# Performance work log

Hardware: AMD Instinct MI355X
Metric: run time of the kernel (lower is better)

The kernel has to match this reference:

```python
import jax, jax.numpy as jnp
import numpy as np

GAMMA = 0.99
LMBDA = 0.95
SHAPE = (8192, 256, 4, 1)  # (batch, steps, agents, 1)


def setup_inputs() -> dict:
    key = jax.random.key(0)
    k1, k2, k3, k4 = jax.random.split(key, 4)
    reward = jax.random.normal(k1, SHAPE, dtype=jnp.float32)
    # sparse binary termination flags (as float, matching terminated.float())
    terminated = (jax.random.uniform(k2, SHAPE) < 0.01).astype(jnp.float32)
    value = jax.random.normal(k3, SHAPE, dtype=jnp.float32)
    next_value = jax.random.normal(k4, SHAPE, dtype=jnp.float32)
    return {"reward": reward, "terminated": terminated,
            "value": value, "next_value": next_value}


def _gae(reward, terminated, value, next_value):
    not_done = 1.0 - terminated
    # delta_t = r_t + gamma * V(s_{t+1}) * not_done_t - V(s_t), all steps at once
    delta = reward + GAMMA * next_value * not_done - value  # (B, T, ...)

    # time-major for the scan: (T, B, ...)
    delta_t = jnp.moveaxis(delta, 1, 0)
    nd_t = jnp.moveaxis(not_done, 1, 0)

    def step(gae, x):
        d, nd = x
        gae = d + GAMMA * LMBDA * nd * gae
        return gae, gae

    init = jnp.zeros(delta_t.shape[1:], dtype=delta.dtype)
    # reverse=True: backward-time recurrence, outputs aligned to original order
    _, adv_t = jax.lax.scan(step, init, (delta_t, nd_t), reverse=True)
    advantages = jnp.moveaxis(adv_t, 0, 1)  # back to (B, T, ...)
    returns = advantages + value
    return advantages, returns


def reference(reward, terminated, value, next_value):
    return _gae(reward, terminated, value, next_value)
```

## Files before the change

kernel.cpp:

```cpp
#include <hip/hip_runtime.h>


#define GAMMA 0.99f
#define LMBDA 0.95f

typedef float f32x4 __attribute__((ext_vector_type(4)));
typedef unsigned char u8;

constexpr float K0 = GAMMA * LMBDA;

__device__ __forceinline__ void issue_loads(
    const f32x4* __restrict__ R4, const f32x4* __restrict__ T4,
    const f32x4* __restrict__ V4, const f32x4* __restrict__ N4,
    int b, int lane, f32x4 r[4], f32x4 tm[4], f32x4 v[4], f32x4 nv[4])
{
#pragma unroll
    for (int q = 0; q < 4; ++q) {
        const int gi = b * 256 + 64 * q + lane;
        r[q]  = R4[gi];
        tm[q] = T4[gi];
        v[q]  = V4[gi];
        nv[q] = N4[gi];
    }
}

__device__ __forceinline__ void phaseA(
    float* __restrict__ D_, u8* __restrict__ C_, int lane,
    const f32x4 r[4], const f32x4 tm[4], const f32x4 nv[4], const f32x4 v[4])
{
#pragma unroll
    for (int q = 0; q < 4; ++q) {
        const int f    = 64 * q + lane;
        const int s    = 255 - f;
        const int row  = s & 15;
        const int col  = (4 * (s >> 4) + 4 * row) & 63;
        const int addr = row * 64 + col;

        f32x4 d4;
        d4.x = r[q].x + GAMMA * nv[q].x * (1.0f - tm[q].x) - v[q].x;
        d4.y = r[q].y + GAMMA * nv[q].y * (1.0f - tm[q].y) - v[q].y;
        d4.z = r[q].z + GAMMA * nv[q].z * (1.0f - tm[q].z) - v[q].z;
        d4.w = r[q].w + GAMMA * nv[q].w * (1.0f - tm[q].w) - v[q].w;
        const unsigned pk = (tm[q].x == 0.0f ? 0x00000001u : 0u)
                          | (tm[q].y == 0.0f ? 0x00000100u : 0u)
                          | (tm[q].z == 0.0f ? 0x00010000u : 0u)
                          | (tm[q].w == 0.0f ? 0x01000000u : 0u);
        *((f32x4*)&D_[addr])    = d4;
        *((unsigned*)&C_[addr]) = pk;
    }
}

__device__ __forceinline__ void scan_store(
    float* __restrict__ D_, const u8* __restrict__ C_,
    int lane, int b, const f32x4 v4[4],
    f32x4* __restrict__ adv4, f32x4* __restrict__ ret4)
{
    asm volatile("s_waitcnt lgkmcnt(0)" ::: "memory");

    const int tc = lane >> 2;
    const int a  = lane & 3;

    float d[16];
    unsigned mask = 0;
#pragma unroll
    for (int j = 0; j < 16; ++j) {
        const int col = (4 * tc + 4 * j + a) & 63;
        d[j] = D_[j * 64 + col];
        mask |= ((unsigned)C_[j * 64 + col]) << j;
    }

    float D = d[0];
    float K = (mask & 1u) ? K0 : 0.0f;
#pragma unroll
    for (int j = 1; j < 16; ++j) {
        const float cj = ((mask >> j) & 1u) ? K0 : 0.0f;
        D = d[j] + cj * D;
        K = cj * K;
    }

#pragma unroll
    for (int s2 = 1; s2 < 16; s2 <<= 1) {
        const float pD = __shfl_up(D, (unsigned)(4 * s2), 64);
        const float pK = __shfl_up(K, (unsigned)(4 * s2), 64);
        if (tc >= s2) { D = D + K * pD; K = K * pK; }
    }

    float x = __shfl_up(D, 4u, 64);
    if (tc == 0) x = 0.0f;

    float g = x;
#pragma unroll
    for (int j = 0; j < 16; ++j) {
        const float cj = ((mask >> j) & 1u) ? K0 : 0.0f;
        g = d[j] + cj * g;
        const int col = (4 * tc + 4 * j + a) & 63;
        D_[j * 64 + col] = g;
    }
    asm volatile("s_waitcnt lgkmcnt(0)" ::: "memory");

#pragma unroll
    for (int q = 0; q < 4; ++q) {
        const int f   = 64 * q + lane;
        const int s   = 255 - f;
        const int row = s & 15;
        const int col = (4 * (s >> 4) + 4 * row) & 63;
        const f32x4 g4 = *((const f32x4*)&D_[row * 64 + col]);

        const int gi = b * 256 + f;
        __builtin_nontemporal_store(g4, &adv4[gi]);
        const f32x4 rt = g4 + v4[q];
        __builtin_nontemporal_store(rt, &ret4[gi]);
    }
    asm volatile("" ::: "memory");
}

__global__ __launch_bounds__(256, 4) void gae_scan_kernel(
    const float* __restrict__ reward,
    const float* __restrict__ terminated,
    const float* __restrict__ value,
    const float* __restrict__ next_value,
    float* __restrict__ adv_out,
    float* __restrict__ ret_out)
{
    __shared__ float bufD[4][16 * 64];
    __shared__ u8    bufC[4][16 * 64];

    const int w    = threadIdx.x >> 6;
    const int lane = threadIdx.x & 63;
    const int wid  = blockIdx.x * 4 + w;

    float* __restrict__ D_ = bufD[w];
    u8*    __restrict__ C_ = bufC[w];

    const f32x4* R4 = (const f32x4*)reward;
    const f32x4* T4 = (const f32x4*)terminated;
    const f32x4* V4 = (const f32x4*)value;
    const f32x4* N4 = (const f32x4*)next_value;
    f32x4* adv4 = (f32x4*)adv_out;
    f32x4* ret4 = (f32x4*)ret_out;

    const int b0 = wid;
    const int b1 = wid + 4096;

    f32x4 r0[4], t0[4], v0[4], n0[4];
    issue_loads(R4, T4, V4, N4, b0, lane, r0, t0, v0, n0);
    phaseA(D_, C_, lane, r0, t0, n0, v0);

    f32x4 r1[4], t1[4], v1[4], n1[4];
    issue_loads(R4, T4, V4, N4, b1, lane, r1, t1, v1, n1);

    scan_store(D_, C_, lane, b0, v0, adv4, ret4);

    phaseA(D_, C_, lane, r1, t1, n1, v1);
    scan_store(D_, C_, lane, b1, v1, adv4, ret4);
}

extern "C" void kernel_launch(void* const* d_in, const int* in_sizes, int n_in,
                              void* d_out, int out_size, void* d_ws, size_t ws_size,
                              hipStream_t stream) {
    const float* reward     = (const float*)d_in[0];
    const float* terminated = (const float*)d_in[1];
    const float* value      = (const float*)d_in[2];
    const float* next_value = (const float*)d_in[3];

    const int B = 8192;
    const int n_elem = B * 256 * 4;
    float* adv = (float*)d_out;
    float* ret = adv + n_elem;

    gae_scan_kernel<<<B / 8, 256, 0, stream>>>(reward, terminated, value,
                                               next_value, adv, ret);
}
```

Baseline: 194.9 us.

## Process four batch rows per wave with double-buffered prefetch and regular stores

Each wave now handles four batch rows instead of two, with a software pipeline that prefetches the next row's inputs into a second register buffer while the current row is scanned. The grid shrinks to 512 blocks and launch bounds relax to 2 blocks per SM so the extra live registers fit. Non-temporal stores are replaced with ordinary stores. This trades occupancy for deeper per-wave latency hiding, and fewer, longer-lived waves may expose more memory latency.

```diff
diff --git a/kernel.cpp b/kernel.cpp
--- a/kernel.cpp
+++ b/kernel.cpp
@@ -107,14 +107,13 @@
         const f32x4 g4 = *((const f32x4*)&D_[row * 64 + col]);
 
         const int gi = b * 256 + f;
-        __builtin_nontemporal_store(g4, &adv4[gi]);
-        const f32x4 rt = g4 + v4[q];
-        __builtin_nontemporal_store(rt, &ret4[gi]);
+        adv4[gi] = g4;
+        ret4[gi] = g4 + v4[q];
     }
     asm volatile("" ::: "memory");
 }
 
-__global__ __launch_bounds__(256, 4) void gae_scan_kernel(
+__global__ __launch_bounds__(256, 2) void gae_scan_kernel(
     const float* __restrict__ reward,
     const float* __restrict__ terminated,
     const float* __restrict__ value,
@@ -127,7 +126,7 @@
 
     const int w    = threadIdx.x >> 6;
     const int lane = threadIdx.x & 63;
-    const int wid  = blockIdx.x * 4 + w;
+    const int wv   = blockIdx.x * 4 + w;
 
     float* __restrict__ D_ = bufD[w];
     u8*    __restrict__ C_ = bufC[w];
@@ -139,20 +138,25 @@
     f32x4* adv4 = (f32x4*)adv_out;
     f32x4* ret4 = (f32x4*)ret_out;
 
-    const int b0 = wid;
-    const int b1 = wid + 4096;
+    f32x4 r[2][4], tm[2][4], v[2][4], nv[2][4];
 
-    f32x4 r0[4], t0[4], v0[4], n0[4];
-    issue_loads(R4, T4, V4, N4, b0, lane, r0, t0, v0, n0);
-    phaseA(D_, C_, lane, r0, t0, n0, v0);
+    issue_loads(R4, T4, V4, N4, wv, lane, r[0], tm[0], v[0], nv[0]);
 
-    f32x4 r1[4], t1[4], v1[4], n1[4];
-    issue_loads(R4, T4, V4, N4, b1, lane, r1, t1, v1, n1);
+#pragma unroll
+    for (int g = 0; g < 4; ++g) {
+        const int cb = g & 1;
+        const int nb = cb ^ 1;
+        const int b  = g * 2048 + wv;
 
-    scan_store(D_, C_, lane, b0, v0, adv4, ret4);
+        phaseA(D_, C_, lane, r[cb], tm[cb], nv[cb], v[cb]);
 
-    phaseA(D_, C_, lane, r1, t1, n1, v1);
-    scan_store(D_, C_, lane, b1, v1, adv4, ret4);
+        if (g < 3) {
+            issue_loads(R4, T4, V4, N4, b + 2048, lane,
+                        r[nb], tm[nb], v[nb], nv[nb]);
+        }
+
+        scan_store(D_, C_, lane, b, v[cb], adv4, ret4);
+    }
 }
 
 extern "C" void kernel_launch(void* const* d_in, const int* in_sizes, int n_in,
@@ -168,6 +172,6 @@
     float* adv = (float*)d_out;
     float* ret = adv + n_elem;
 
-    gae_scan_kernel<<<B / 8, 256, 0, stream>>>(reward, terminated, value,
-                                               next_value, adv, ret);
+    gae_scan_kernel<<<512, 256, 0, stream>>>(reward, terminated, value,
+                                             next_value, adv, ret);
 }
```

Measured after the change: 176.5 us. -9.5%, faster.
